# Optimization experiments

Hardware: AMD Instinct MI355X
Metric: run time of the kernel (lower is better)

Reference implementation:

```python
import jax, jax.numpy as jnp
import numpy as np

B, S, A, MSG, C = 524288, 64, 16, 32, 4
CH = 9 + S  # children_states feature dim = 73
EPS = 1e-12  # F.normalize clamp_min eps


def _l2norm(v):
    n = jnp.sqrt(jnp.sum(v * v, axis=-1, keepdims=True))
    return v / jnp.maximum(n, EPS)


def setup_inputs() -> dict:
    key = jax.random.key(0)
    ks = jax.random.split(key, 12)
    def lin(kw, kb, out_d, in_d):
        bound = 1.0 / np.sqrt(in_d)
        W = jax.random.uniform(kw, (out_d, in_d), minval=-bound, maxval=bound, dtype=jnp.float32)
        b = jax.random.uniform(kb, (out_d,), minval=-bound, maxval=bound, dtype=jnp.float32)
        return W, b
    W1, b1 = lin(ks[0], ks[1], 64, S + A)
    W2, b2 = lin(ks[2], ks[3], 64, 64 + MSG)
    W3, b3 = lin(ks[4], ks[5], MSG, 64)
    Wa, ba = lin(ks[6], ks[7], MSG, CH)
    return {
        "x": jax.random.normal(ks[8], (B, S), dtype=jnp.float32),
        "u": jax.random.normal(ks[9], (B, A), dtype=jnp.float32),
        "children_states": jax.random.normal(ks[10], (B, C, CH), dtype=jnp.float32),
        "m": jax.random.normal(ks[11], (B, C * MSG), dtype=jnp.float32),
        "W1": W1, "b1": b1, "W2": W2, "b2": b2, "W3": W3, "b3": b3,
        "Wa": Wa, "ba": ba,
    }


def reference(x, u, children_states, m, W1, b1, W2, b2, W3, b3, Wa, ba):
    # fc1 on cat(x, u), then L2 normalize
    xu = jnp.concatenate([x, u], axis=-1) @ W1.T + b1          # [B, 64]
    xu = _l2norm(xu)
    # attention over children (softmax along child axis, dim=-2)
    att = jax.nn.softmax(children_states @ Wa.T + ba, axis=-2)  # [B, C, MSG]
    mm = m.reshape(*children_states.shape[:-1], -1)             # [B, C, MSG]
    magg = jnp.sum(mm * att, axis=-2)                           # [B, MSG]
    # fused MLP tail
    xum = jnp.tanh(jnp.concatenate([xu, magg], axis=-1))        # [B, 64+MSG]
    xum = jnp.tanh(xum @ W2.T + b2)                             # [B, 64]
    xum = xum @ W3.T + b3                                       # [B, MSG]
    return _l2norm(xum)
```

## Files before the change

### kernel.cpp

```cpp
#include <hip/hip_runtime.h>
#include <cstddef>

typedef __fp16 f16x8 __attribute__((ext_vector_type(8)));
typedef float f32x4 __attribute__((ext_vector_type(4)));
typedef unsigned int uint32;
typedef unsigned short ushort;

constexpr int S = 64, MSG = 32, CH = 73;

constexpr int FC1_OFF = 0;
constexpr int ATT_OFF = 12 * 512;
constexpr int FC2_OFF = 18 * 512;
constexpr int FC3_OFF = 30 * 512;
constexpr int WS_ELEMS = 34 * 512;

__global__ void prep_pack(const float* __restrict__ W1, const float* __restrict__ b1,
                          const float* __restrict__ Wa, const float* __restrict__ ba,
                          const float* __restrict__ W2, const float* __restrict__ W3,
                          ushort* __restrict__ wsf) {
  int idx = blockIdx.x * 256 + threadIdx.x;
  if (idx >= WS_ELEMS) return;
  int tile = idx >> 9;
  int lane = (idx >> 3) & 63;
  int e = idx & 7;
  int jloc = lane & 15;
  int kloc = ((lane >> 4) << 3) + e;
  float v = 0.f;
  if (tile < 12) {
    int t = tile >> 2, f = tile & 3;
    int j = f * 16 + jloc, k = t * 32 + kloc;
    v = (k < 80) ? W1[j * 80 + k] : (k == 80 ? b1[j] : 0.f);
  } else if (tile < 18) {
    int q = tile - 12, t = q >> 1, f = q & 1;
    int j = f * 16 + jloc, k = t * 32 + kloc;
    v = (k < 73) ? Wa[j * 73 + k] : (k == 73 ? ba[j] : 0.f);
  } else if (tile < 30) {
    int q = tile - 18, t = q >> 2, f = q & 3;
    int j = f * 16 + jloc, k = t * 32 + kloc;
    v = W2[j * 96 + k];
  } else {
    int q = tile - 30, t = q >> 1, f = q & 1;
    int j = f * 16 + jloc, k = t * 32 + kloc;
    v = W3[j * 64 + k];
  }
  union { __fp16 h; ushort s; } cv;
  cv.h = (__fp16)v;
  wsf[idx] = cv.s;
}

__device__ __forceinline__ f32x4 mf(f16x8 a, f16x8 b, f32x4 c) {
  return __builtin_amdgcn_mfma_f32_16x16x32_f16(a, b, c, 0, 0, 0);
}
__device__ __forceinline__ uint32 pku(float a, float b) {
  auto r = __builtin_amdgcn_cvt_pkrtz(a, b);
  union { decltype(r) f; uint32 u; } v; v.f = r; return v.u;
}
__device__ __forceinline__ f16x8 packA(const float* f) {
  union { uint32 u[4]; f16x8 h; } r;
  r.u[0] = pku(f[0], f[1]); r.u[1] = pku(f[2], f[3]);
  r.u[2] = pku(f[4], f[5]); r.u[3] = pku(f[6], f[7]);
  return r.h;
}
__device__ __forceinline__ f16x8 packA2(float4 a, float4 b) {
  union { uint32 u[4]; f16x8 h; } r;
  r.u[0] = pku(a.x, a.y); r.u[1] = pku(a.z, a.w);
  r.u[2] = pku(b.x, b.y); r.u[3] = pku(b.z, b.w);
  return r.h;
}
__device__ __forceinline__ float fast_tanh(float v) {
  v = fminf(15.f, fmaxf(-15.f, v));
  float t = __expf(2.f * v);
  return (t - 1.f) * __builtin_amdgcn_rcpf(t + 1.f);
}

constexpr int HT_LD = 104;
constexpr int H2_LD = 72;

__launch_bounds__(256)
__global__ void critic_mfma_kernel(
    const float* __restrict__ x, const float* __restrict__ u,
    const float* __restrict__ cs, const float* __restrict__ m,
    const float* __restrict__ b2, const float* __restrict__ b3,
    const ushort* __restrict__ wsf, float* __restrict__ out, int n) {
  __shared__ __attribute__((aligned(16))) float csb[4][1168];
  __shared__ __attribute__((aligned(16))) __fp16 hbuf[4][16 * HT_LD];
  __shared__ __attribute__((aligned(16))) __fp16 h2buf[4][16 * H2_LD];

  const int wave = threadIdx.x >> 6;
  const int lane = threadIdx.x & 63;
  const int lm = lane & 15;
  const int lq = lane >> 4;
  const int r0 = (blockIdx.x * 4 + wave) * 16;
  if (r0 >= n) return;

  float* __restrict__ csw = &csb[wave][0];
  __fp16* __restrict__ ht = &hbuf[wave][0];
  __fp16* __restrict__ h2t = &h2buf[wave][0];

  const float4* __restrict__ xrow4 =
      reinterpret_cast<const float4*>(x + (size_t)(r0 + lm) * S);
  float4 xva = xrow4[2 * lq], xvb = xrow4[2 * lq + 1];
  float4 xvc = xrow4[8 + 2 * lq], xvd = xrow4[9 + 2 * lq];
  const int uq = (lq < 2) ? lq : 0;
  const float4* __restrict__ urow4 =
      reinterpret_cast<const float4*>(u + (size_t)(r0 + lm) * 16);
  float4 uva = urow4[2 * uq], uvb = urow4[2 * uq + 1];

  auto ldB = [&](int off_tile) -> f16x8 {
    return *reinterpret_cast<const f16x8*>(wsf + off_tile + lane * 8);
  };

  f16x8 wa[6];
#pragma unroll
  for (int i = 0; i < 6; ++i) wa[i] = ldB(ATT_OFF + i * 512);

#pragma unroll
  for (int g = 0; g < 4; ++g) {
    {
      const float4* __restrict__ src =
          reinterpret_cast<const float4*>(cs + (size_t)(r0 * 4 + 16 * g) * CH);
      float4* __restrict__ dst = reinterpret_cast<float4*>(csw);
#pragma unroll
      for (int i = 0; i < 4; ++i) dst[i * 64 + lane] = src[i * 64 + lane];
      if (lane < 36) dst[256 + lane] = src[256 + lane];
    }
    const float* __restrict__ crow = csw + lm * CH;
    f32x4 zac[2] = {{0.f, 0.f, 0.f, 0.f}, {0.f, 0.f, 0.f, 0.f}};
#pragma unroll
    for (int t = 0; t < 3; ++t) {
      float f[8];
      const int kbase = t * 32 + lq * 8;
#pragma unroll
      for (int e = 0; e < 8; ++e) {
        int k = kbase + e;
        f[e] = (k < 73) ? crow[k] : (k == 73 ? 1.f : 0.f);
      }
      f16x8 af = packA(f);
      zac[0] = mf(af, wa[t * 2 + 0], zac[0]);
      zac[1] = mf(af, wa[t * 2 + 1], zac[1]);
    }
    const int bo = r0 + 4 * g + lq;
    const float* __restrict__ mrow = m + (size_t)bo * 128;
#pragma unroll
    for (int f = 0; f < 2; ++f) {
      const int j = lm + 16 * f;
      float e0 = __expf(zac[f][0]);
      float e1 = __expf(zac[f][1]);
      float e2 = __expf(zac[f][2]);
      float e3 = __expf(zac[f][3]);
      float den = (e0 + e1) + (e2 + e3);
      float num = fmaf(mrow[0 * 32 + j], e0,
                  fmaf(mrow[1 * 32 + j], e1,
                  fmaf(mrow[2 * 32 + j], e2, mrow[3 * 32 + j] * e3)));
      float mg = num * __builtin_amdgcn_rcpf(den);
      ht[(4 * g + lq) * HT_LD + 64 + j] = (__fp16)fast_tanh(mg);
    }
  }

  f32x4 hac[4] = {{0.f,0.f,0.f,0.f},{0.f,0.f,0.f,0.f},{0.f,0.f,0.f,0.f},{0.f,0.f,0.f,0.f}};
  {
    f16x8 a0 = packA2(xva, xvb);
    f16x8 a1 = packA2(xvc, xvd);
#pragma unroll
    for (int fi = 0; fi < 4; ++fi) hac[fi] = mf(a0, ldB(FC1_OFF + fi * 512), hac[fi]);
#pragma unroll
    for (int fi = 0; fi < 4; ++fi) hac[fi] = mf(a1, ldB(FC1_OFF + (4 + fi) * 512), hac[fi]);
    float f[8];
    float uf[8] = {uva.x, uva.y, uva.z, uva.w, uvb.x, uvb.y, uvb.z, uvb.w};
#pragma unroll
    for (int e = 0; e < 8; ++e) {
      int k = 64 + lq * 8 + e;
      f[e] = (k < 80) ? ((lq < 2) ? uf[e] : 0.f) : (k == 80 ? 1.f : 0.f);
    }
    f16x8 a2f = packA(f);
#pragma unroll
    for (int fi = 0; fi < 4; ++fi) hac[fi] = mf(a2f, ldB(FC1_OFF + (8 + fi) * 512), hac[fi]);
  }
  {
    float rn[4];
#pragma unroll
    for (int reg = 0; reg < 4; ++reg) {
      float s = hac[0][reg] * hac[0][reg];
      s = fmaf(hac[1][reg], hac[1][reg], s);
      s = fmaf(hac[2][reg], hac[2][reg], s);
      s = fmaf(hac[3][reg], hac[3][reg], s);
      s += __shfl_xor(s, 1);
      s += __shfl_xor(s, 2);
      s += __shfl_xor(s, 4);
      s += __shfl_xor(s, 8);
      rn[reg] = __builtin_amdgcn_rcpf(fmaxf(sqrtf(s), 1e-12f));
    }
#pragma unroll
    for (int fi = 0; fi < 4; ++fi)
#pragma unroll
      for (int reg = 0; reg < 4; ++reg)
        ht[(4 * lq + reg) * HT_LD + lm + 16 * fi] =
            (__fp16)fast_tanh(hac[fi][reg] * rn[reg]);
  }

  {
    f32x4 ac2[4] = {{0.f,0.f,0.f,0.f},{0.f,0.f,0.f,0.f},{0.f,0.f,0.f,0.f},{0.f,0.f,0.f,0.f}};
    f16x8 a2[3];
#pragma unroll
    for (int t = 0; t < 3; ++t)
      a2[t] = *reinterpret_cast<const f16x8*>(ht + lm * HT_LD + t * 32 + lq * 8);
#pragma unroll
    for (int t = 0; t < 3; ++t)
#pragma unroll
      for (int fi = 0; fi < 4; ++fi)
        ac2[fi] = mf(a2[t], ldB(FC2_OFF + (t * 4 + fi) * 512), ac2[fi]);
#pragma unroll
    for (int fi = 0; fi < 4; ++fi) {
      float bv = b2[lm + 16 * fi];
#pragma unroll
      for (int reg = 0; reg < 4; ++reg)
        h2t[(4 * lq + reg) * H2_LD + lm + 16 * fi] =
            (__fp16)fast_tanh(ac2[fi][reg] + bv);
    }
  }

  {
    f32x4 o[2] = {{0.f,0.f,0.f,0.f},{0.f,0.f,0.f,0.f}};
    f16x8 a3[2];
#pragma unroll
    for (int t = 0; t < 2; ++t)
      a3[t] = *reinterpret_cast<const f16x8*>(h2t + lm * H2_LD + t * 32 + lq * 8);
#pragma unroll
    for (int t = 0; t < 2; ++t)
#pragma unroll
      for (int fi = 0; fi < 2; ++fi)
        o[fi] = mf(a3[t], ldB(FC3_OFF + (t * 2 + fi) * 512), o[fi]);
#pragma unroll
    for (int fi = 0; fi < 2; ++fi) {
      float bv = b3[lm + 16 * fi];
#pragma unroll
      for (int reg = 0; reg < 4; ++reg) o[fi][reg] += bv;
    }
    float rn2[4];
#pragma unroll
    for (int reg = 0; reg < 4; ++reg) {
      float s = fmaf(o[0][reg], o[0][reg], o[1][reg] * o[1][reg]);
      s += __shfl_xor(s, 1);
      s += __shfl_xor(s, 2);
      s += __shfl_xor(s, 4);
      s += __shfl_xor(s, 8);
      rn2[reg] = __builtin_amdgcn_rcpf(fmaxf(sqrtf(s), 1e-12f));
    }
#pragma unroll
    for (int fi = 0; fi < 2; ++fi)
#pragma unroll
      for (int reg = 0; reg < 4; ++reg)
        out[(size_t)(r0 + 4 * lq + reg) * MSG + lm + 16 * fi] =
            o[fi][reg] * rn2[reg];
  }
}

extern "C" void kernel_launch(void* const* d_in, const int* in_sizes, int n_in,
                              void* d_out, int out_size, void* d_ws, size_t ws_size,
                              hipStream_t stream) {
  const float* x  = (const float*)d_in[0];
  const float* u  = (const float*)d_in[1];
  const float* cs = (const float*)d_in[2];
  const float* m  = (const float*)d_in[3];
  const float* W1 = (const float*)d_in[4];
  const float* b1 = (const float*)d_in[5];
  const float* W2 = (const float*)d_in[6];
  const float* b2 = (const float*)d_in[7];
  const float* W3 = (const float*)d_in[8];
  const float* b3 = (const float*)d_in[9];
  const float* Wa = (const float*)d_in[10];
  const float* ba = (const float*)d_in[11];
  float* out = (float*)d_out;
  ushort* wsf = (ushort*)d_ws;

  const int n = in_sizes[0] / S;

  hipLaunchKernelGGL(prep_pack, dim3((WS_ELEMS + 255) / 256), dim3(256), 0, stream,
                     W1, b1, Wa, ba, W2, W3, wsf);

  const int blocks = (n + 63) / 64;
  hipLaunchKernelGGL(critic_mfma_kernel, dim3(blocks), dim3(256), 0, stream,
                     x, u, cs, m, b2, b3, wsf, out, n);
}
```

Before: 231.7 us.

## Prefetch next children_states chunk into registers and alias csb with h2buf

```diff
diff --git a/kernel.cpp b/kernel.cpp
--- a/kernel.cpp
+++ b/kernel.cpp
@@ -75,6 +75,10 @@
 
 constexpr int HT_LD = 104;
 constexpr int H2_LD = 72;
+constexpr int HBUF_B = 3328;
+constexpr int UNION_OFF = 13312;
+constexpr int UNION_B = 4672;
+constexpr int SMEM_B = 32000;
 
 __launch_bounds__(256)
 __global__ void critic_mfma_kernel(
@@ -82,9 +86,7 @@
     const float* __restrict__ cs, const float* __restrict__ m,
     const float* __restrict__ b2, const float* __restrict__ b3,
     const ushort* __restrict__ wsf, float* __restrict__ out, int n) {
-  __shared__ __attribute__((aligned(16))) float csb[4][1168];
-  __shared__ __attribute__((aligned(16))) __fp16 hbuf[4][16 * HT_LD];
-  __shared__ __attribute__((aligned(16))) __fp16 h2buf[4][16 * H2_LD];
+  __shared__ __attribute__((aligned(16))) unsigned char smem[SMEM_B];
 
   const int wave = threadIdx.x >> 6;
   const int lane = threadIdx.x & 63;
@@ -93,9 +95,9 @@
   const int r0 = (blockIdx.x * 4 + wave) * 16;
   if (r0 >= n) return;
 
-  float* __restrict__ csw = &csb[wave][0];
-  __fp16* __restrict__ ht = &hbuf[wave][0];
-  __fp16* __restrict__ h2t = &h2buf[wave][0];
+  __fp16* __restrict__ ht = reinterpret_cast<__fp16*>(smem + wave * HBUF_B);
+  float* __restrict__ csw = reinterpret_cast<float*>(smem + UNION_OFF + wave * UNION_B);
+  __fp16* __restrict__ h2t = reinterpret_cast<__fp16*>(smem + UNION_OFF + wave * UNION_B);
 
   const float4* __restrict__ xrow4 =
       reinterpret_cast<const float4*>(x + (size_t)(r0 + lm) * S);
@@ -114,15 +116,38 @@
 #pragma unroll
   for (int i = 0; i < 6; ++i) wa[i] = ldB(ATT_OFF + i * 512);
 
+  float4 csr0, csr1, csr2, csr3, csr4;
+  {
+    const float4* __restrict__ src =
+        reinterpret_cast<const float4*>(cs + (size_t)(r0 * 4) * CH);
+    csr0 = src[lane];       csr1 = src[64 + lane];
+    csr2 = src[128 + lane]; csr3 = src[192 + lane];
+    if (lane < 36) csr4 = src[256 + lane];
+  }
+
 #pragma unroll
   for (int g = 0; g < 4; ++g) {
     {
+      float4* __restrict__ dst = reinterpret_cast<float4*>(csw);
+      dst[lane] = csr0;       dst[64 + lane] = csr1;
+      dst[128 + lane] = csr2; dst[192 + lane] = csr3;
+      if (lane < 36) dst[256 + lane] = csr4;
+    }
+    float mr[8];
+    {
+      const float* __restrict__ mrow = m + (size_t)(r0 + 4 * g + lq) * 128;
+#pragma unroll
+      for (int c = 0; c < 4; ++c) {
+        mr[c * 2 + 0] = mrow[c * 32 + lm];
+        mr[c * 2 + 1] = mrow[c * 32 + lm + 16];
+      }
+    }
+    if (g < 3) {
       const float4* __restrict__ src =
-          reinterpret_cast<const float4*>(cs + (size_t)(r0 * 4 + 16 * g) * CH);
-      float4* __restrict__ dst = reinterpret_cast<float4*>(csw);
-#pragma unroll
-      for (int i = 0; i < 4; ++i) dst[i * 64 + lane] = src[i * 64 + lane];
-      if (lane < 36) dst[256 + lane] = src[256 + lane];
+          reinterpret_cast<const float4*>(cs + (size_t)(r0 * 4 + 16 * (g + 1)) * CH);
+      csr0 = src[lane];       csr1 = src[64 + lane];
+      csr2 = src[128 + lane]; csr3 = src[192 + lane];
+      if (lane < 36) csr4 = src[256 + lane];
     }
     const float* __restrict__ crow = csw + lm * CH;
     f32x4 zac[2] = {{0.f, 0.f, 0.f, 0.f}, {0.f, 0.f, 0.f, 0.f}};
@@ -139,8 +164,6 @@
       zac[0] = mf(af, wa[t * 2 + 0], zac[0]);
       zac[1] = mf(af, wa[t * 2 + 1], zac[1]);
     }
-    const int bo = r0 + 4 * g + lq;
-    const float* __restrict__ mrow = m + (size_t)bo * 128;
 #pragma unroll
     for (int f = 0; f < 2; ++f) {
       const int j = lm + 16 * f;
@@ -149,9 +172,9 @@
       float e2 = __expf(zac[f][2]);
       float e3 = __expf(zac[f][3]);
       float den = (e0 + e1) + (e2 + e3);
-      float num = fmaf(mrow[0 * 32 + j], e0,
-                  fmaf(mrow[1 * 32 + j], e1,
-                  fmaf(mrow[2 * 32 + j], e2, mrow[3 * 32 + j] * e3)));
+      float num = fmaf(mr[0 * 2 + f], e0,
+                  fmaf(mr[1 * 2 + f], e1,
+                  fmaf(mr[2 * 2 + f], e2, mr[3 * 2 + f] * e3)));
       float mg = num * __builtin_amdgcn_rcpf(den);
       ht[(4 * g + lq) * HT_LD + 64 + j] = (__fp16)fast_tanh(mg);
     }
```

After: 223.8 us. -3.4%, faster.

## Double-buffer children_states via direct global-to-LDS loads with manual waitcnt pipelining

Applied to the files above, without the earlier changes.

```diff
diff --git a/kernel.cpp b/kernel.cpp
--- a/kernel.cpp
+++ b/kernel.cpp
@@ -73,8 +73,19 @@
   return (t - 1.f) * __builtin_amdgcn_rcpf(t + 1.f);
 }
 
+__device__ __forceinline__ void gload16(const float* g, void* l) {
+  __builtin_amdgcn_global_load_lds(
+      (const __attribute__((address_space(1))) void*)g,
+      (__attribute__((address_space(3))) void*)l, 16, 0, 0);
+}
+
 constexpr int HT_LD = 104;
 constexpr int H2_LD = 72;
+constexpr int HBUF_B = 3328;
+constexpr int CS_B = 4672;
+constexpr int CSA_OFF = 4 * HBUF_B;
+constexpr int CSB_OFF = CSA_OFF + 4 * CS_B;
+constexpr int SMEM_B = CSB_OFF + 4 * CS_B;
 
 __launch_bounds__(256)
 __global__ void critic_mfma_kernel(
@@ -82,9 +93,7 @@
     const float* __restrict__ cs, const float* __restrict__ m,
     const float* __restrict__ b2, const float* __restrict__ b3,
     const ushort* __restrict__ wsf, float* __restrict__ out, int n) {
-  __shared__ __attribute__((aligned(16))) float csb[4][1168];
-  __shared__ __attribute__((aligned(16))) __fp16 hbuf[4][16 * HT_LD];
-  __shared__ __attribute__((aligned(16))) __fp16 h2buf[4][16 * H2_LD];
+  __shared__ __attribute__((aligned(16))) unsigned char smem[SMEM_B];
 
   const int wave = threadIdx.x >> 6;
   const int lane = threadIdx.x & 63;
@@ -93,10 +102,39 @@
   const int r0 = (blockIdx.x * 4 + wave) * 16;
   if (r0 >= n) return;
 
-  float* __restrict__ csw = &csb[wave][0];
-  __fp16* __restrict__ ht = &hbuf[wave][0];
-  __fp16* __restrict__ h2t = &h2buf[wave][0];
-
+  __fp16* __restrict__ ht = reinterpret_cast<__fp16*>(smem + wave * HBUF_B);
+  unsigned char* __restrict__ csAb = smem + CSA_OFF + wave * CS_B;
+  unsigned char* __restrict__ csBb = smem + CSB_OFF + wave * CS_B;
+  const float* __restrict__ csAf = reinterpret_cast<const float*>(csAb);
+  const float* __restrict__ csBf = reinterpret_cast<const float*>(csBb);
+  __fp16* __restrict__ h2t = reinterpret_cast<__fp16*>(csAb);
+
+  auto ldB = [&](int off_tile) -> f16x8 {
+    return *reinterpret_cast<const f16x8*>(wsf + off_tile + lane * 8);
+  };
+
+  auto gloadChunk = [&](int row16, unsigned char* buf) {
+    const float* sl = cs + (size_t)row16 * CH + lane * 4;
+    gload16(sl,        buf);
+    gload16(sl + 256,  buf + 1024);
+    gload16(sl + 512,  buf + 2048);
+    gload16(sl + 768,  buf + 3072);
+    if (lane < 36) gload16(sl + 1024, buf + 4096);
+  };
+  float MA[8], MB[8];
+  auto issueM = [&](float* MR, int g) {
+    const float* __restrict__ mrow = m + (size_t)(r0 + 4 * g + lq) * 128;
+#pragma unroll
+    for (int c = 0; c < 4; ++c) {
+      MR[c * 2 + 0] = mrow[c * 32 + lm];
+      MR[c * 2 + 1] = mrow[c * 32 + lm + 16];
+    }
+  };
+
+  f16x8 wa[6];
+#pragma unroll
+  for (int i = 0; i < 6; ++i) wa[i] = ldB(ATT_OFF + i * 512);
+  __builtin_amdgcn_sched_barrier(0);
   const float4* __restrict__ xrow4 =
       reinterpret_cast<const float4*>(x + (size_t)(r0 + lm) * S);
   float4 xva = xrow4[2 * lq], xvb = xrow4[2 * lq + 1];
@@ -105,42 +143,43 @@
   const float4* __restrict__ urow4 =
       reinterpret_cast<const float4*>(u + (size_t)(r0 + lm) * 16);
   float4 uva = urow4[2 * uq], uvb = urow4[2 * uq + 1];
-
-  auto ldB = [&](int off_tile) -> f16x8 {
-    return *reinterpret_cast<const f16x8*>(wsf + off_tile + lane * 8);
-  };
-
-  f16x8 wa[6];
-#pragma unroll
-  for (int i = 0; i < 6; ++i) wa[i] = ldB(ATT_OFF + i * 512);
+  __builtin_amdgcn_sched_barrier(0);
+  gloadChunk(r0 * 4, csAb);
+  __builtin_amdgcn_sched_barrier(0);
+  issueM(MA, 0);
+  __builtin_amdgcn_sched_barrier(0);
+  gloadChunk(r0 * 4 + 16, csBb);
+  __builtin_amdgcn_sched_barrier(0);
 
 #pragma unroll
   for (int g = 0; g < 4; ++g) {
-    {
-      const float4* __restrict__ src =
-          reinterpret_cast<const float4*>(cs + (size_t)(r0 * 4 + 16 * g) * CH);
-      float4* __restrict__ dst = reinterpret_cast<float4*>(csw);
-#pragma unroll
-      for (int i = 0; i < 4; ++i) dst[i * 64 + lane] = src[i * 64 + lane];
-      if (lane < 36) dst[256 + lane] = src[256 + lane];
-    }
-    const float* __restrict__ crow = csw + lm * CH;
+    if (g == 3) { asm volatile("s_waitcnt vmcnt(8)" ::: "memory"); }
+    else        { asm volatile("s_waitcnt vmcnt(13)" ::: "memory"); }
+    __builtin_amdgcn_sched_barrier(0);
+
+    const float* __restrict__ crow = ((g & 1) ? csBf : csAf) + lm * CH;
     f32x4 zac[2] = {{0.f, 0.f, 0.f, 0.f}, {0.f, 0.f, 0.f, 0.f}};
 #pragma unroll
-    for (int t = 0; t < 3; ++t) {
+    for (int tt = 0; tt < 3; ++tt) {
       float f[8];
-      const int kbase = t * 32 + lq * 8;
+      const int kbase = tt * 32 + lq * 8;
 #pragma unroll
       for (int e = 0; e < 8; ++e) {
         int k = kbase + e;
         f[e] = (k < 73) ? crow[k] : (k == 73 ? 1.f : 0.f);
       }
       f16x8 af = packA(f);
-      zac[0] = mf(af, wa[t * 2 + 0], zac[0]);
-      zac[1] = mf(af, wa[t * 2 + 1], zac[1]);
-    }
-    const int bo = r0 + 4 * g + lq;
-    const float* __restrict__ mrow = m + (size_t)bo * 128;
+      zac[0] = mf(af, wa[tt * 2 + 0], zac[0]);
+      zac[1] = mf(af, wa[tt * 2 + 1], zac[1]);
+    }
+    asm volatile("s_waitcnt lgkmcnt(0)" ::: "memory");
+    __builtin_amdgcn_sched_barrier(0);
+    if (g < 2) gloadChunk(r0 * 4 + 16 * (g + 2), (g & 1) ? csBb : csAb);
+    __builtin_amdgcn_sched_barrier(0);
+    if (g < 3) issueM((g & 1) ? MA : MB, g + 1);
+    __builtin_amdgcn_sched_barrier(0);
+
+    const float* MR = (g & 1) ? MB : MA;
 #pragma unroll
     for (int f = 0; f < 2; ++f) {
       const int j = lm + 16 * f;
@@ -149,9 +188,9 @@
       float e2 = __expf(zac[f][2]);
       float e3 = __expf(zac[f][3]);
       float den = (e0 + e1) + (e2 + e3);
-      float num = fmaf(mrow[0 * 32 + j], e0,
-                  fmaf(mrow[1 * 32 + j], e1,
-                  fmaf(mrow[2 * 32 + j], e2, mrow[3 * 32 + j] * e3)));
+      float num = fmaf(MR[0 + f], e0,
+                  fmaf(MR[2 + f], e1,
+                  fmaf(MR[4 + f], e2, MR[6 + f] * e3)));
       float mg = num * __builtin_amdgcn_rcpf(den);
       ht[(4 * g + lq) * HT_LD + 64 + j] = (__fp16)fast_tanh(mg);
     }
@@ -161,10 +200,6 @@
   {
     f16x8 a0 = packA2(xva, xvb);
     f16x8 a1 = packA2(xvc, xvd);
-#pragma unroll
-    for (int fi = 0; fi < 4; ++fi) hac[fi] = mf(a0, ldB(FC1_OFF + fi * 512), hac[fi]);
-#pragma unroll
-    for (int fi = 0; fi < 4; ++fi) hac[fi] = mf(a1, ldB(FC1_OFF + (4 + fi) * 512), hac[fi]);
     float f[8];
     float uf[8] = {uva.x, uva.y, uva.z, uva.w, uvb.x, uvb.y, uvb.z, uvb.w};
 #pragma unroll
@@ -173,6 +208,10 @@
       f[e] = (k < 80) ? ((lq < 2) ? uf[e] : 0.f) : (k == 80 ? 1.f : 0.f);
     }
     f16x8 a2f = packA(f);
+#pragma unroll
+    for (int fi = 0; fi < 4; ++fi) hac[fi] = mf(a0, ldB(FC1_OFF + fi * 512), hac[fi]);
+#pragma unroll
+    for (int fi = 0; fi < 4; ++fi) hac[fi] = mf(a1, ldB(FC1_OFF + (4 + fi) * 512), hac[fi]);
 #pragma unroll
     for (int fi = 0; fi < 4; ++fi) hac[fi] = mf(a2f, ldB(FC1_OFF + (8 + fi) * 512), hac[fi]);
   }
@@ -202,13 +241,13 @@
     f32x4 ac2[4] = {{0.f,0.f,0.f,0.f},{0.f,0.f,0.f,0.f},{0.f,0.f,0.f,0.f},{0.f,0.f,0.f,0.f}};
     f16x8 a2[3];
 #pragma unroll
-    for (int t = 0; t < 3; ++t)
-      a2[t] = *reinterpret_cast<const f16x8*>(ht + lm * HT_LD + t * 32 + lq * 8);
-#pragma unroll
-    for (int t = 0; t < 3; ++t)
+    for (int tt = 0; tt < 3; ++tt)
+      a2[tt] = *reinterpret_cast<const f16x8*>(ht + lm * HT_LD + tt * 32 + lq * 8);
+#pragma unroll
+    for (int tt = 0; tt < 3; ++tt)
 #pragma unroll
       for (int fi = 0; fi < 4; ++fi)
-        ac2[fi] = mf(a2[t], ldB(FC2_OFF + (t * 4 + fi) * 512), ac2[fi]);
+        ac2[fi] = mf(a2[tt], ldB(FC2_OFF + (tt * 4 + fi) * 512), ac2[fi]);
 #pragma unroll
     for (int fi = 0; fi < 4; ++fi) {
       float bv = b2[lm + 16 * fi];
@@ -223,13 +262,13 @@
     f32x4 o[2] = {{0.f,0.f,0.f,0.f},{0.f,0.f,0.f,0.f}};
     f16x8 a3[2];
 #pragma unroll
-    for (int t = 0; t < 2; ++t)
-      a3[t] = *reinterpret_cast<const f16x8*>(h2t + lm * H2_LD + t * 32 + lq * 8);
-#pragma unroll
-    for (int t = 0; t < 2; ++t)
+    for (int tt = 0; tt < 2; ++tt)
+      a3[tt] = *reinterpret_cast<const f16x8*>(h2t + lm * H2_LD + tt * 32 + lq * 8);
+#pragma unroll
+    for (int tt = 0; tt < 2; ++tt)
 #pragma unroll
       for (int fi = 0; fi < 2; ++fi)
-        o[fi] = mf(a3[t], ldB(FC3_OFF + (t * 2 + fi) * 512), o[fi]);
+        o[fi] = mf(a3[tt], ldB(FC3_OFF + (tt * 2 + fi) * 512), o[fi]);
 #pragma unroll
     for (int fi = 0; fi < 2; ++fi) {
       float bv = b3[lm + 16 * fi];
```

Result: faster. 220.6 us (-4.8%).
